# Performance work log

Hardware: AMD Instinct MI355X
Metric: run time of the kernel (lower is better)

## Reference

```python
import jax, jax.numpy as jnp
import numpy as np

B, T, DIM, H, HD = 2, 2048, 1024, 8, 128
ATTN_SCALE = 0.12  # attn_args.attn_scale (modded-nanogpt constant)
F32_EPS = float(np.finfo(np.float32).eps)  # F.rms_norm default eps


def ste_round(x):
    # straight-through round (round_grad_pt): identity gradient
    return x + jax.lax.stop_gradient(jnp.round(x) - x)


def quantized_linear(x, num_bits=8, eps=1e-5):
    num_steps = (2 ** num_bits - 1) // 2  # 127
    xnmin = jnp.minimum(jnp.min(x, -1, keepdims=True), -eps)
    xpmax = jnp.maximum(jnp.max(x, -1, keepdims=True), eps)
    xp = ste_round(x / xpmax * num_steps) / num_steps * xpmax
    xn = ste_round(x / xnmin * num_steps) / num_steps * xnmin
    return jnp.where(x >= 0, xp, xn)


def ternary_quantize_mean_special(w):
    # w: [3, hdim, dim]; per-leading-slice scale
    s = jnp.maximum(jnp.mean(jnp.mean(jnp.abs(w), -1, keepdims=True), -2, keepdims=True), 1e-5)
    return s * jnp.clip(ste_round(w / s), -1.0, 1.0)


def ternary_quantize(w):
    s = jnp.maximum(jnp.mean(jnp.abs(w)), 1e-5)
    return s * jnp.clip(ste_round(w / s), -1.0, 1.0)


def rmsnorm(x):
    return x * jax.lax.rsqrt(jnp.mean(x * x, -1, keepdims=True) + F32_EPS)


def rotary(x, cos, sin):
    # x: [B,T,H,HD]; cos,sin: [T, HD//2]
    x1, x2 = jnp.split(x, 2, axis=-1)
    c = cos[None, :, None, :]
    s = sin[None, :, None, :]
    return jnp.concatenate([x1 * c + x2 * s, -x1 * s + x2 * c], axis=-1)


def setup_inputs() -> dict:
    key = jax.random.key(0)
    ks = jax.random.split(key, 5)
    x = jax.random.normal(ks[0], (B, T, DIM), jnp.float32)
    ve = jax.random.normal(ks[1], (B, T, DIM), jnp.float32)
    sa_lambdas = jnp.array([0.5, 0.5], jnp.float32)
    inv_freq = 1.0 / (10000.0 ** (np.arange(0, HD, 2, dtype=np.float32) / HD))
    ang = np.arange(T, dtype=np.float32)[:, None] * inv_freq[None, :]
    cos = jnp.asarray(np.cos(ang), jnp.float32)
    sin = jnp.asarray(np.sin(ang), jnp.float32)
    bound = (3.0 ** 0.5) * 0.5 * DIM ** (-0.5)
    qkvo_w = jax.random.uniform(ks[2], (4, H * HD, DIM), jnp.float32, -bound, bound)
    gate_w = 0.1 * jax.random.normal(ks[3], (H, 12), jnp.float32)
    return {"x": x, "ve": ve, "sa_lambdas": sa_lambdas, "cos": cos, "sin": sin,
            "qkvo_w": qkvo_w, "gate_w": gate_w}


def reference(x, ve, sa_lambdas, cos, sin, qkvo_w, gate_w):
    # pre-activation int8 fake-quant (ENABLE_ATTN_PRE_ACT_QUANTIZATION)
    xq = quantized_linear(x, num_bits=8)
    # ternary-quantized QKV weights (ENABLE_ATTN_QUANTIZATION)
    w_qkv = ternary_quantize_mean_special(qkvo_w[:3]).reshape(3 * H * HD, DIM)
    qkv = jnp.einsum('btd,ed->bte', xq, w_qkv).reshape(B, T, 3 * H, HD)
    q, k, v = qkv[:, :, :H], qkv[:, :, H:2 * H], qkv[:, :, 2 * H:]
    q, k = rmsnorm(q), rmsnorm(k)
    q, k = rotary(q, cos, sin), rotary(k, cos, sin)
    v = sa_lambdas[0] * v + sa_lambdas[1] * ve.reshape(v.shape)
    # q/k int8 fake-quant (ENABLE_ATTN_ACT_QUANTIZATION)
    q = quantized_linear(q, num_bits=8)
    k = quantized_linear(k, num_bits=8)
    # causal SDPA with explicit scale
    scores = jnp.einsum('bqhd,bkhd->bhqk', q, k) * ATTN_SCALE
    mask = jnp.tril(jnp.ones((T, T), bool))
    scores = jnp.where(mask[None, None], scores, -jnp.inf)
    p = jax.nn.softmax(scores, axis=-1)
    y = jnp.einsum('bhqk,bkhd->bqhd', p, v)  # [B,T,H,HD]
    # sigmoid gate from first 12 features of (quantized) x
    gate = jax.nn.sigmoid(jnp.einsum('btf,hf->bth', xq[..., :12], gate_w))
    y = (y * gate[..., None]).reshape(B, T, H * HD)
    # ternary-quantized output projection (ENABLE_ATTN_PROJ_QUANTIZATION)
    w_o = ternary_quantize(qkvo_w[3])
    return jnp.einsum('bte,de->btd', y, w_o)
```

## Files before the change

kernel.cpp:

```cpp
#include <hip/hip_runtime.h>
#include <hip/hip_bf16.h>
#include <cstddef>
#include <cstdint>

#define B_    2
#define T_    2048
#define DIM_  1024
#define H_    8
#define HD_   128
#define BT_   (B_*T_)
#define E3_   (3*H_*HD_)
#define F32_EPS_ 1.1920929e-07f

typedef __attribute__((ext_vector_type(8))) short bh8_t;
typedef __attribute__((ext_vector_type(4))) float f32x4_t;
typedef __attribute__((ext_vector_type(16))) float f32x16_t;
typedef __attribute__((ext_vector_type(4))) unsigned short us4_t;

__device__ inline unsigned short bf16r(float f) {
    unsigned u = __builtin_bit_cast(unsigned, f);
    u = (u + 0x7fffu + ((u >> 16) & 1u)) >> 16;
    return (unsigned short)u;
}
__device__ inline unsigned bf16pk(float a, float b) {
    return (unsigned)bf16r(a) | ((unsigned)bf16r(b) << 16);
}
__device__ inline void gl16(const unsigned short* g, unsigned short* l) {
    __builtin_amdgcn_global_load_lds((const __attribute__((address_space(1))) void*)g,
                                     (__attribute__((address_space(3))) void*)l, 16, 0, 0);
}

__global__ __launch_bounds__(256) void absmean1_kernel(const float* __restrict__ w, float* __restrict__ partial) {
    int blk = blockIdx.x;
    size_t off = (size_t)blk * 4096;
    __shared__ float red[256];
    int tid = threadIdx.x;
    float acc = 0.f;
    const float* p = w + off + tid*16;
    #pragma unroll
    for (int j = 0; j < 4; j++) {
        float4 v = *(const float4*)(p + j*4);
        acc += fabsf(v.x) + fabsf(v.y) + fabsf(v.z) + fabsf(v.w);
    }
    red[tid] = acc; __syncthreads();
    for (int s = 128; s > 0; s >>= 1) { if (tid < s) red[tid] += red[tid+s]; __syncthreads(); }
    if (tid == 0) partial[blk] = red[0];
}

__global__ __launch_bounds__(256) void absmean2_kernel(const float* __restrict__ partial, float* __restrict__ scales) {
    int m = blockIdx.x;
    __shared__ float red[256];
    int tid = threadIdx.x;
    red[tid] = partial[m*256 + tid]; __syncthreads();
    for (int s = 128; s > 0; s >>= 1) { if (tid < s) red[tid] += red[tid+s]; __syncthreads(); }
    if (tid == 0) scales[m] = fmaxf(red[0] / (float)(DIM_*DIM_), 1e-5f);
}

__global__ __launch_bounds__(256) void quant_w_kernel(const float* __restrict__ w, const float* __restrict__ scales,
                                                      unsigned short* __restrict__ wq) {
    int base = (blockIdx.x * 256 + threadIdx.x) * 8;
    float s = scales[base >> 20];
    float inv = 1.f / s;
    unsigned short out[8];
    float4 v0 = *(const float4*)(w + base);
    float4 v1 = *(const float4*)(w + base + 4);
    float t[8] = {v0.x, v0.y, v0.z, v0.w, v1.x, v1.y, v1.z, v1.w};
    #pragma unroll
    for (int j = 0; j < 8; j++) {
        float r = rintf(t[j] * inv);
        r = fminf(1.f, fmaxf(-1.f, r));
        out[j] = (r == 0.f) ? 0 : (r > 0.f ? 0x3F80 : 0xBF80);
    }
    *(int4*)(wq + base) = *(const int4*)out;
}

__global__ __launch_bounds__(256) void quant_x_gate_kernel(const float* __restrict__ x, const float* __restrict__ gw,
                                                           unsigned short* __restrict__ xqb, float* __restrict__ gate) {
    int row = blockIdx.x;
    const float* xr = x + (size_t)row * DIM_;
    unsigned short* qr = xqb + (size_t)row * DIM_;
    __shared__ float red[256];
    __shared__ float x12[12];
    int tid = threadIdx.x;
    float v[4];
    float mn = 1e30f, mx = -1e30f;
    #pragma unroll
    for (int i = 0; i < 4; i++) {
        v[i] = xr[i*256 + tid];
        mn = fminf(mn, v[i]); mx = fmaxf(mx, v[i]);
    }
    red[tid] = mn; __syncthreads();
    for (int s = 128; s > 0; s >>= 1) { if (tid < s) red[tid] = fminf(red[tid], red[tid+s]); __syncthreads(); }
    mn = red[0]; __syncthreads();
    red[tid] = mx; __syncthreads();
    for (int s = 128; s > 0; s >>= 1) { if (tid < s) red[tid] = fmaxf(red[tid], red[tid+s]); __syncthreads(); }
    mx = red[0]; __syncthreads();
    float p = fmaxf(mx, 1e-5f);
    float n = fminf(mn, -1e-5f);
    #pragma unroll
    for (int i = 0; i < 4; i++) {
        int gi = i*256 + tid;
        float xv = v[i];
        float sc = (xv >= 0.f) ? p : n;
        float q = rintf(xv / sc * 127.f) / 127.f * sc;
        qr[gi] = bf16r(q);
        if (gi < 12) x12[gi] = q;
    }
    __syncthreads();
    if (tid < H_) {
        float acc = 0.f;
        #pragma unroll
        for (int f = 0; f < 12; f++) acc += x12[f] * gw[tid*12 + f];
        gate[(size_t)row * H_ + tid] = 1.f / (1.f + expf(-acc));
    }
}

__global__ __launch_bounds__(256) void gemm_bf16_kernel(const unsigned short* __restrict__ A,
                                                        const unsigned short* __restrict__ Bm,
                                                        const float* __restrict__ sw, int sbase,
                                                        float* __restrict__ C, int M, int N, int K) {
    __shared__ __align__(16) unsigned short As[128*64];
    __shared__ __align__(16) unsigned short Bs[128*64];
    int bm = blockIdx.y * 128, bn = blockIdx.x * 128;
    int tid = threadIdx.x;
    int w = tid >> 6, l = tid & 63;
    int wr = w >> 1, wc = w & 1;
    int lg = l >> 4, lq = l & 15;
    f32x4_t acc[4][4];
    #pragma unroll
    for (int mt = 0; mt < 4; mt++)
        #pragma unroll
        for (int nt = 0; nt < 4; nt++) acc[mt][nt] = (f32x4_t)0.f;

    for (int k0 = 0; k0 < K; k0 += 64) {
        #pragma unroll
        for (int i = 0; i < 4; i++) {
            int ob = (i*4 + w) << 10;
            int o  = ob + (l << 4);
            int row = o >> 7;
            int scn = (o >> 4) & 7;
            int lcn = scn ^ (row & 7);
            gl16(A  + (size_t)(bm+row)*K + k0 + lcn*8, (unsigned short*)As + (ob >> 1));
            gl16(Bm + (size_t)(bn+row)*K + k0 + lcn*8, (unsigned short*)Bs + (ob >> 1));
        }
        __syncthreads();
        #pragma unroll
        for (int kk = 0; kk < 2; kk++) {
            bh8_t af[4], bf[4];
            #pragma unroll
            for (int mt = 0; mt < 4; mt++) {
                int r = wr*64 + mt*16 + lq;
                int j = kk*4 + lg;
                af[mt] = *(const bh8_t*)(As + r*64 + (((j ^ (r & 7)))<<3));
            }
            #pragma unroll
            for (int nt = 0; nt < 4; nt++) {
                int r = wc*64 + nt*16 + lq;
                int j = kk*4 + lg;
                bf[nt] = *(const bh8_t*)(Bs + r*64 + (((j ^ (r & 7)))<<3));
            }
            #pragma unroll
            for (int mt = 0; mt < 4; mt++)
                #pragma unroll
                for (int nt = 0; nt < 4; nt++)
                    acc[mt][nt] = __builtin_amdgcn_mfma_f32_16x16x32_bf16(af[mt], bf[nt], acc[mt][nt], 0, 0, 0);
        }
        __syncthreads();
    }
    #pragma unroll
    for (int nt = 0; nt < 4; nt++) {
        int col = bn + wc*64 + nt*16 + lq;
        float s = sw[sbase + (col >> 10)];
        #pragma unroll
        for (int mt = 0; mt < 4; mt++) {
            int row = bm + wr*64 + mt*16 + lg*4;
            #pragma unroll
            for (int r = 0; r < 4; r++)
                C[(size_t)(row + r)*N + col] = acc[mt][nt][r] * s;
        }
    }
}

__global__ __launch_bounds__(256) void qkv_post_kernel(const float* __restrict__ qkv, const float* __restrict__ ve,
                                                       const float* __restrict__ lam,
                                                       const float* __restrict__ cosb, const float* __restrict__ sinb,
                                                       unsigned short* __restrict__ Qb, unsigned short* __restrict__ Kb,
                                                       unsigned short* __restrict__ Vb) {
    int bt = blockIdx.x;
    int b = bt >> 11, t = bt & (T_ - 1);
    int w = threadIdx.x >> 6, l = threadIdx.x & 63;
    const float* base = qkv + (size_t)bt * E3_;
    float l0 = lam[0], l1 = lam[1];
    #pragma unroll
    for (int i = 0; i < 2; i++) {
        int h = w*2 + i;
        const float* row = base + (16 + h)*HD_;
        const float* ver = ve + (size_t)bt*DIM_ + h*HD_;
        unsigned short* dst = Vb + ((size_t)(b*H_+h)*T_ + t)*HD_;
        dst[l]      = bf16r(l0*row[l]    + l1*ver[l]);
        dst[l + 64] = bf16r(l0*row[l+64] + l1*ver[l+64]);
    }
    float cc = cosb[(size_t)t*64 + l], ss = sinb[(size_t)t*64 + l];
    #pragma unroll
    for (int i = 0; i < 4; i++) {
        int part = w*4 + i;
        const float* row = base + part*HD_;
        float x1 = row[l], x2 = row[l+64];
        float ssq = x1*x1 + x2*x2;
        #pragma unroll
        for (int off = 1; off < 64; off <<= 1) ssq += __shfl_xor(ssq, off);
        float rms = 1.0f / sqrtf(ssq / 128.0f + F32_EPS_);
        x1 *= rms; x2 *= rms;
        float o1 = x1*cc + x2*ss;
        float o2 = -x1*ss + x2*cc;
        float mn = fminf(o1, o2), mx = fmaxf(o1, o2);
        #pragma unroll
        for (int off = 1; off < 64; off <<= 1) {
            mn = fminf(mn, __shfl_xor(mn, off));
            mx = fmaxf(mx, __shfl_xor(mx, off));
        }
        float p = fmaxf(mx, 1e-5f);
        float n = fminf(mn, -1e-5f);
        float s1 = (o1 >= 0.f) ? p : n;
        float s2 = (o2 >= 0.f) ? p : n;
        float q1 = rintf(o1 / s1 * 127.f) / 127.f * s1;
        float q2 = rintf(o2 / s2 * 127.f) / 127.f * s2;
        if (part < 8) {
            unsigned short* dst = Qb + ((size_t)(b*H_+part)*T_ + t)*HD_;
            dst[l] = bf16r(0.12f * q1); dst[l + 64] = bf16r(0.12f * q2);
        } else {
            unsigned short* dst = Kb + ((size_t)(b*H_+part-8)*T_ + t)*HD_;
            dst[l] = bf16r(q1); dst[l + 64] = bf16r(q2);
        }
    }
}

__global__ __launch_bounds__(256) void transpose_v_kernel(const unsigned short* __restrict__ Vb,
                                                          unsigned short* __restrict__ VT) {
    int tt = blockIdx.x;
    int dt = blockIdx.y;
    int bh = blockIdx.z;
    __shared__ unsigned short L[64][80];
    int tid = threadIdx.x;
    #pragma unroll
    for (int i = 0; i < 2; i++) {
        int c = tid + i*256;
        int r = c >> 3, dc = c & 7;
        int4 v = *(const int4*)(Vb + ((size_t)bh*T_ + tt*64 + r)*HD_ + dt*64 + dc*8);
        *(int4*)(&L[r][dc*8]) = v;
    }
    __syncthreads();
    #pragma unroll
    for (int i = 0; i < 2; i++) {
        int c = tid + i*256;
        int r = c >> 3, tc = c & 7;
        unsigned short tmp[8];
        #pragma unroll
        for (int jj = 0; jj < 8; jj++) tmp[jj] = L[tc*8+jj][r];
        *(int4*)(VT + ((size_t)bh*HD_ + dt*64 + r)*T_ + tt*64 + tc*8) = *(const int4*)tmp;
    }
}

__global__ __launch_bounds__(256) void attn_kernel(const unsigned short* __restrict__ Qb,
                                                   const unsigned short* __restrict__ Kb,
                                                   const unsigned short* __restrict__ VT,
                                                   const float* __restrict__ gate,
                                                   unsigned short* __restrict__ Yb) {
    __shared__ __align__(16) unsigned char SMEM[65536];
    int id = blockIdx.x;
    int bh = id & 15;
    int qi = id >> 4;
    int qt = (qi < 16) ? (31 - qi) : (qi - 16);
    int b = bh >> 3, h = bh & 7;
    int tid = threadIdx.x;
    int w = tid >> 6, l = tid & 63;
    int qsub = w >> 1, qq = w & 1;
    int hh = l >> 5, l5 = l & 31;
    int qrow = qsub*32 + l5;
    int qg = qt*64 + qrow;

    const unsigned short* Kbase = Kb + (size_t)bh*T_*HD_;
    const unsigned short* Vbase = VT + (size_t)bh*HD_*T_;
    const unsigned short* Qg = Qb + ((size_t)bh*T_ + (size_t)qt*64) * HD_;

    bh8_t qf[8];
    #pragma unroll
    for (int ks = 0; ks < 8; ks++)
        qf[ks] = *(const bh8_t*)(Qg + (size_t)qrow*HD_ + ks*16 + hh*8);

    int nr = qt + 1;

    f32x16_t o0 = (f32x16_t)0.f, o1 = (f32x16_t)0.f, o2 = (f32x16_t)0.f, o3 = (f32x16_t)0.f;
    float mrun = -1e20f, lrun = 0.f;

#define STAGE(BI, J) { \
    unsigned short* kb_ = (unsigned short*)(SMEM + (BI)*16384); \
    unsigned short* vb_ = (unsigned short*)(SMEM + 32768 + (BI)*16384); \
    _Pragma("unroll") \
    for (int i_ = 0; i_ < 4; i_++) { \
        int ob_ = (i_*4 + w) << 10; \
        int o_  = ob_ + (l << 4); \
        int rk_ = o_ >> 8; \
        int lk_ = ((o_ >> 4) & 15) ^ (rk_ & 7); \
        gl16(Kbase + (size_t)((J)*64 + rk_)*HD_ + lk_*8, kb_ + (ob_ >> 1)); \
        int rv_ = o_ >> 7; \
        int lv_ = ((o_ >> 4) & 7) ^ (rv_ & 7); \
        gl16(Vbase + (size_t)rv_*T_ + (J)*64 + lv_*8, vb_ + (ob_ >> 1)); \
    } }

    STAGE(0, 0);
    for (int j = 0; j < nr; j++) {
        if (j + 1 < nr) {
            STAGE((j+1) & 1, j+1);
            asm volatile("s_waitcnt vmcnt(8)" ::: "memory");
        } else {
            asm volatile("s_waitcnt vmcnt(0)" ::: "memory");
        }
        __builtin_amdgcn_s_barrier();
        asm volatile("" ::: "memory");
        const unsigned short* kb = (const unsigned short*)(SMEM + (j&1)*16384);
        const unsigned short* vb = (const unsigned short*)(SMEM + 32768 + (j&1)*16384);
        int kvb = j*64 + qq*32;
        if (kvb <= qt*64 + qsub*32 + 31) {
            f32x16_t s = (f32x16_t)0.f;
            int krow = qq*32 + l5;
            #pragma unroll
            for (int ks = 0; ks < 8; ks++) {
                int c = (ks*2 + hh) ^ (krow & 7);
                bh8_t kf = *(const bh8_t*)(kb + krow*128 + c*8);
                s = __builtin_amdgcn_mfma_f32_32x32x16_bf16(kf, qf[ks], s, 0, 0, 0);
            }
            if (kvb + 31 > qt*64 + qsub*32) {
                #pragma unroll
                for (int r = 0; r < 16; r++) {
                    int key = kvb + (r & 3) + 8*(r >> 2) + 4*hh;
                    if (key > qg) s[r] = -1e30f;
                }
            }
            float tm = s[0];
            #pragma unroll
            for (int r = 1; r < 16; r++) tm = fmaxf(tm, s[r]);
            tm = fmaxf(tm, __shfl_xor(tm, 32));
            if (!__all(tm - mrun <= 8.f)) {
                float mnew = fmaxf(mrun, tm);
                float scf = __expf(mrun - mnew);
                lrun *= scf;
                o0 *= scf; o1 *= scf; o2 *= scf; o3 *= scf;
                mrun = mnew;
            }
            float p[16]; float ls = 0.f;
            #pragma unroll
            for (int r = 0; r < 16; r++) { p[r] = __expf(s[r] - mrun); ls += p[r]; }
            ls += __shfl_xor(ls, 32);
            lrun += ls;
            unsigned u0 = bf16pk(p[0], p[1]),   u1 = bf16pk(p[2], p[3]);
            unsigned u2 = bf16pk(p[4], p[5]),   u3 = bf16pk(p[6], p[7]);
            unsigned u4 = bf16pk(p[8], p[9]),   u5 = bf16pk(p[10], p[11]);
            unsigned u6 = bf16pk(p[12], p[13]), u7 = bf16pk(p[14], p[15]);
            unsigned x0 = (unsigned)__shfl_xor((int)u0, 32), x1 = (unsigned)__shfl_xor((int)u1, 32);
            unsigned x2 = (unsigned)__shfl_xor((int)u2, 32), x3 = (unsigned)__shfl_xor((int)u3, 32);
            unsigned x4 = (unsigned)__shfl_xor((int)u4, 32), x5 = (unsigned)__shfl_xor((int)u5, 32);
            unsigned x6 = (unsigned)__shfl_xor((int)u6, 32), x7 = (unsigned)__shfl_xor((int)u7, 32);
            union { bh8_t v; unsigned uu[4]; } B0, B1;
            B0.uu[0] = hh ? x2 : u0;  B0.uu[1] = hh ? x3 : u1;
            B0.uu[2] = hh ? u2 : x0;  B0.uu[3] = hh ? u3 : x1;
            B1.uu[0] = hh ? x6 : u4;  B1.uu[1] = hh ? x7 : u5;
            B1.uu[2] = hh ? u6 : x4;  B1.uu[3] = hh ? u7 : x5;
#define PV_STEP(DT, OACC) { \
    int vrow = DT*32 + l5; \
    bh8_t vf0 = *(const bh8_t*)(vb + vrow*64 + (((qq*4 + hh) ^ (vrow & 7))<<3)); \
    OACC = __builtin_amdgcn_mfma_f32_32x32x16_bf16(vf0, B0.v, OACC, 0, 0, 0); \
    bh8_t vf1 = *(const bh8_t*)(vb + vrow*64 + (((qq*4 + 2 + hh) ^ (vrow & 7))<<3)); \
    OACC = __builtin_amdgcn_mfma_f32_32x32x16_bf16(vf1, B1.v, OACC, 0, 0, 0); }
            PV_STEP(0, o0) PV_STEP(1, o1) PV_STEP(2, o2) PV_STEP(3, o3)
#undef PV_STEP
        }
        asm volatile("s_waitcnt lgkmcnt(0)" ::: "memory");
        __builtin_amdgcn_s_barrier();
        asm volatile("" ::: "memory");
    }

    f32x16_t oA[4] = {o0, o1, o2, o3};
    float* OB = (float*)SMEM;
    float* ML = (float*)(SMEM + 32768);
    unsigned short* YS = (unsigned short*)(SMEM + 33280);
    if (qq != 0) {
        float* obuf = OB + (size_t)qsub * 4096;
        #pragma unroll
        for (int dt = 0; dt < 4; dt++)
            #pragma unroll
            for (int g = 0; g < 4; g++) {
                f32x4_t v4;
                #pragma unroll
                for (int e = 0; e < 4; e++) v4[e] = oA[dt][g*4+e];
                int ch = (dt*4 + g) ^ (l & 7);
                *(f32x4_t*)(obuf + l*64 + ch*4) = v4;
            }
        if (hh == 0) {
            ML[(qsub*32 + l5)*2]     = mrun;
            ML[(qsub*32 + l5)*2 + 1] = lrun;
        }
    }
    __syncthreads();
    if (qq == 0) {
        float mb = ML[(qsub*32 + l5)*2];
        float lb = ML[(qsub*32 + l5)*2 + 1];
        float mN = fmaxf(mrun, mb);
        float fa = __expf(mrun - mN), fb = __expf(mb - mN);
        const float* obuf = OB + (size_t)qsub * 4096;
        #pragma unroll
        for (int dt = 0; dt < 4; dt++)
            #pragma unroll
            for (int g = 0; g < 4; g++) {
                int ch = (dt*4 + g) ^ (l & 7);
                f32x4_t v4 = *(const f32x4_t*)(obuf + l*64 + ch*4);
                #pragma unroll
                for (int e = 0; e < 4; e++)
                    oA[dt][g*4+e] = oA[dt][g*4+e]*fa + v4[e]*fb;
            }
        lrun = lrun*fa + lb*fb;
        float gv = gate[((size_t)b*T_ + (size_t)qg)*H_ + h];
        float inv = gv / lrun;
        #pragma unroll
        for (int dt = 0; dt < 4; dt++)
            #pragma unroll
            for (int g = 0; g < 4; g++) {
                unsigned short pk4[4];
                #pragma unroll
                for (int e = 0; e < 4; e++) pk4[e] = bf16r(oA[dt][g*4+e] * inv);
                int ch = (dt*4 + g) ^ (qrow & 7);
                *(us4_t*)(YS + (size_t)qrow*128 + ch*8 + hh*4) = *(const us4_t*)pk4;
            }
    }
    __syncthreads();
    #pragma unroll
    for (int i = 0; i < 4; i++) {
        int idx = tid + i*256;
        int r = idx >> 4, scn = idx & 15;
        int lcn = scn ^ (r & 7);
        int4 v = *(const int4*)(YS + (size_t)r*128 + scn*8);
        *(int4*)(Yb + (size_t)(b*T_ + qt*64 + r)*DIM_ + h*HD_ + lcn*8) = v;
    }
#undef STAGE
}

extern "C" void kernel_launch(void* const* d_in, const int* in_sizes, int n_in,
                              void* d_out, int out_size, void* d_ws, size_t ws_size,
                              hipStream_t stream) {
    const float* x    = (const float*)d_in[0];
    const float* ve   = (const float*)d_in[1];
    const float* lam  = (const float*)d_in[2];
    const float* cosb = (const float*)d_in[3];
    const float* sinb = (const float*)d_in[4];
    const float* qkvo = (const float*)d_in[5];
    const float* gw   = (const float*)d_in[6];

    char* ws = (char*)d_ws;
    float* scales  = (float*)ws;
    float* partial = scales + 16;
    unsigned short* WQb = (unsigned short*)(ws + (1<<13));
    unsigned short* XQb = WQb + (size_t)4*DIM_*DIM_;
    float* QKV = (float*)(XQb + (size_t)BT_*DIM_);
    float* GT  = QKV + (size_t)BT_*E3_;
    unsigned short* Qb = (unsigned short*)(GT + (size_t)BT_*H_);
    unsigned short* Kb = Qb + (size_t)B_*H_*T_*HD_;
    unsigned short* VT = Kb + (size_t)B_*H_*T_*HD_;
    unsigned short* Vb = VT + (size_t)B_*H_*T_*HD_;
    unsigned short* Yb = (unsigned short*)QKV;

    absmean1_kernel<<<1024, 256, 0, stream>>>(qkvo, partial);
    absmean2_kernel<<<4, 256, 0, stream>>>(partial, scales);
    quant_w_kernel<<<(4*DIM_*DIM_)/(256*8), 256, 0, stream>>>(qkvo, scales, WQb);
    quant_x_gate_kernel<<<BT_, 256, 0, stream>>>(x, gw, XQb, GT);
    gemm_bf16_kernel<<<dim3(E3_/128, BT_/128), 256, 0, stream>>>(XQb, WQb, scales, 0, QKV, BT_, E3_, DIM_);
    qkv_post_kernel<<<BT_, 256, 0, stream>>>(QKV, ve, lam, cosb, sinb, Qb, Kb, Vb);
    transpose_v_kernel<<<dim3(T_/64, HD_/64, B_*H_), 256, 0, stream>>>(Vb, VT);
    attn_kernel<<<512, 256, 0, stream>>>(Qb, Kb, VT, GT, Yb);
    gemm_bf16_kernel<<<dim3(DIM_/128, BT_/128), 256, 0, stream>>>(Yb, WQb + (size_t)3*DIM_*DIM_, scales, 3,
                                                                  (float*)d_out, BT_, DIM_, DIM_);
}
```

Measured before the change: 152.5 us.

## Store QKV in bf16, use exp2 softmax, retile output GEMM, add setprio

The QKV GEMM now writes bf16 instead of fp32, which halves the intermediate traffic between it and the post-processing kernel. The attention softmax moves to exp2 by folding log2(e) into the Q scale, uses tree reductions and a hardware packed bf16 convert, and raises wave priority around the MFMA sections. The K LDS swizzle is widened to 16 chunks to reduce bank conflicts. The output projection uses 64-row tiles to launch more blocks. Rounding QKV to bf16 before the RMS norm adds precision loss.

Result: faster. 145.8 us (-4.4%).

```diff
diff --git a/kernel.cpp b/kernel.cpp
--- a/kernel.cpp
+++ b/kernel.cpp
@@ -11,6 +11,7 @@
 #define BT_   (B_*T_)
 #define E3_   (3*H_*HD_)
 #define F32_EPS_ 1.1920929e-07f
+#define QSC_  0.17312340490667562f
 
 typedef __attribute__((ext_vector_type(8))) short bh8_t;
 typedef __attribute__((ext_vector_type(4))) float f32x4_t;
@@ -22,8 +23,13 @@
     u = (u + 0x7fffu + ((u >> 16) & 1u)) >> 16;
     return (unsigned short)u;
 }
-__device__ inline unsigned bf16pk(float a, float b) {
-    return (unsigned)bf16r(a) | ((unsigned)bf16r(b) << 16);
+__device__ inline float b2f(unsigned short u) {
+    return __builtin_bit_cast(float, (unsigned)u << 16);
+}
+__device__ inline unsigned cvtpk(float a, float b) {
+    unsigned r;
+    asm("v_cvt_pk_bf16_f32 %0, %1, %2" : "=v"(r) : "v"(a), "v"(b));
+    return r;
 }
 __device__ inline void gl16(const unsigned short* g, unsigned short* l) {
     __builtin_amdgcn_global_load_lds((const __attribute__((address_space(1))) void*)g,
@@ -115,41 +121,48 @@
     }
 }
 
+template<int MT, bool OBF>
 __global__ __launch_bounds__(256) void gemm_bf16_kernel(const unsigned short* __restrict__ A,
                                                         const unsigned short* __restrict__ Bm,
                                                         const float* __restrict__ sw, int sbase,
-                                                        float* __restrict__ C, int M, int N, int K) {
-    __shared__ __align__(16) unsigned short As[128*64];
+                                                        void* __restrict__ Cv, int M, int N, int K) {
+    __shared__ __align__(16) unsigned short As[MT*32*64];
     __shared__ __align__(16) unsigned short Bs[128*64];
-    int bm = blockIdx.y * 128, bn = blockIdx.x * 128;
+    int bm = blockIdx.y * (MT*32), bn = blockIdx.x * 128;
     int tid = threadIdx.x;
     int w = tid >> 6, l = tid & 63;
     int wr = w >> 1, wc = w & 1;
     int lg = l >> 4, lq = l & 15;
-    f32x4_t acc[4][4];
-    #pragma unroll
-    for (int mt = 0; mt < 4; mt++)
+    f32x4_t acc[MT][4];
+    #pragma unroll
+    for (int mt = 0; mt < MT; mt++)
         #pragma unroll
         for (int nt = 0; nt < 4; nt++) acc[mt][nt] = (f32x4_t)0.f;
 
     for (int k0 = 0; k0 < K; k0 += 64) {
+        #pragma unroll
+        for (int i = 0; i < MT; i++) {
+            int ob = (i*4 + w) << 10;
+            int o  = ob + (l << 4);
+            int row = o >> 7;
+            int lcn = ((o >> 4) & 7) ^ (row & 7);
+            gl16(A + (size_t)(bm+row)*K + k0 + lcn*8, (unsigned short*)As + (ob >> 1));
+        }
         #pragma unroll
         for (int i = 0; i < 4; i++) {
             int ob = (i*4 + w) << 10;
             int o  = ob + (l << 4);
             int row = o >> 7;
-            int scn = (o >> 4) & 7;
-            int lcn = scn ^ (row & 7);
-            gl16(A  + (size_t)(bm+row)*K + k0 + lcn*8, (unsigned short*)As + (ob >> 1));
+            int lcn = ((o >> 4) & 7) ^ (row & 7);
             gl16(Bm + (size_t)(bn+row)*K + k0 + lcn*8, (unsigned short*)Bs + (ob >> 1));
         }
         __syncthreads();
         #pragma unroll
         for (int kk = 0; kk < 2; kk++) {
-            bh8_t af[4], bf[4];
-            #pragma unroll
-            for (int mt = 0; mt < 4; mt++) {
-                int r = wr*64 + mt*16 + lq;
+            bh8_t af[MT], bf[4];
+            #pragma unroll
+            for (int mt = 0; mt < MT; mt++) {
+                int r = wr*(MT*16) + mt*16 + lq;
                 int j = kk*4 + lg;
                 af[mt] = *(const bh8_t*)(As + r*64 + (((j ^ (r & 7)))<<3));
             }
@@ -160,7 +173,7 @@
                 bf[nt] = *(const bh8_t*)(Bs + r*64 + (((j ^ (r & 7)))<<3));
             }
             #pragma unroll
-            for (int mt = 0; mt < 4; mt++)
+            for (int mt = 0; mt < MT; mt++)
                 #pragma unroll
                 for (int nt = 0; nt < 4; nt++)
                     acc[mt][nt] = __builtin_amdgcn_mfma_f32_16x16x32_bf16(af[mt], bf[nt], acc[mt][nt], 0, 0, 0);
@@ -172,16 +185,21 @@
         int col = bn + wc*64 + nt*16 + lq;
         float s = sw[sbase + (col >> 10)];
         #pragma unroll
-        for (int mt = 0; mt < 4; mt++) {
-            int row = bm + wr*64 + mt*16 + lg*4;
-            #pragma unroll
-            for (int r = 0; r < 4; r++)
-                C[(size_t)(row + r)*N + col] = acc[mt][nt][r] * s;
-        }
-    }
-}
-
-__global__ __launch_bounds__(256) void qkv_post_kernel(const float* __restrict__ qkv, const float* __restrict__ ve,
+        for (int mt = 0; mt < MT; mt++) {
+            int row = bm + wr*(MT*16) + mt*16 + lg*4;
+            #pragma unroll
+            for (int r = 0; r < 4; r++) {
+                if constexpr (OBF)
+                    ((unsigned short*)Cv)[(size_t)(row + r)*N + col] = bf16r(acc[mt][nt][r] * s);
+                else
+                    ((float*)Cv)[(size_t)(row + r)*N + col] = acc[mt][nt][r] * s;
+            }
+        }
+    }
+}
+
+__global__ __launch_bounds__(256) void qkv_post_kernel(const unsigned short* __restrict__ qkvb,
+                                                       const float* __restrict__ ve,
                                                        const float* __restrict__ lam,
                                                        const float* __restrict__ cosb, const float* __restrict__ sinb,
                                                        unsigned short* __restrict__ Qb, unsigned short* __restrict__ Kb,
@@ -189,23 +207,23 @@
     int bt = blockIdx.x;
     int b = bt >> 11, t = bt & (T_ - 1);
     int w = threadIdx.x >> 6, l = threadIdx.x & 63;
-    const float* base = qkv + (size_t)bt * E3_;
+    const unsigned short* base = qkvb + (size_t)bt * E3_;
     float l0 = lam[0], l1 = lam[1];
     #pragma unroll
     for (int i = 0; i < 2; i++) {
         int h = w*2 + i;
-        const float* row = base + (16 + h)*HD_;
+        const unsigned short* row = base + (16 + h)*HD_;
         const float* ver = ve + (size_t)bt*DIM_ + h*HD_;
         unsigned short* dst = Vb + ((size_t)(b*H_+h)*T_ + t)*HD_;
-        dst[l]      = bf16r(l0*row[l]    + l1*ver[l]);
-        dst[l + 64] = bf16r(l0*row[l+64] + l1*ver[l+64]);
+        dst[l]      = bf16r(l0*b2f(row[l])    + l1*ver[l]);
+        dst[l + 64] = bf16r(l0*b2f(row[l+64]) + l1*ver[l+64]);
     }
     float cc = cosb[(size_t)t*64 + l], ss = sinb[(size_t)t*64 + l];
     #pragma unroll
     for (int i = 0; i < 4; i++) {
         int part = w*4 + i;
-        const float* row = base + part*HD_;
-        float x1 = row[l], x2 = row[l+64];
+        const unsigned short* row = base + part*HD_;
+        float x1 = b2f(row[l]), x2 = b2f(row[l+64]);
         float ssq = x1*x1 + x2*x2;
         #pragma unroll
         for (int off = 1; off < 64; off <<= 1) ssq += __shfl_xor(ssq, off);
@@ -227,7 +245,7 @@
         float q2 = rintf(o2 / s2 * 127.f) / 127.f * s2;
         if (part < 8) {
             unsigned short* dst = Qb + ((size_t)(b*H_+part)*T_ + t)*HD_;
-            dst[l] = bf16r(0.12f * q1); dst[l + 64] = bf16r(0.12f * q2);
+            dst[l] = bf16r(QSC_ * q1); dst[l + 64] = bf16r(QSC_ * q2);
         } else {
             unsigned short* dst = Kb + ((size_t)(b*H_+part-8)*T_ + t)*HD_;
             dst[l] = bf16r(q1); dst[l + 64] = bf16r(q2);
@@ -301,7 +319,7 @@
         int ob_ = (i_*4 + w) << 10; \
         int o_  = ob_ + (l << 4); \
         int rk_ = o_ >> 8; \
-        int lk_ = ((o_ >> 4) & 15) ^ (rk_ & 7); \
+        int lk_ = ((o_ >> 4) & 15) ^ (rk_ & 15); \
         gl16(Kbase + (size_t)((J)*64 + rk_)*HD_ + lk_*8, kb_ + (ob_ >> 1)); \
         int rv_ = o_ >> 7; \
         int lv_ = ((o_ >> 4) & 7) ^ (rv_ & 7); \
@@ -324,12 +342,14 @@
         if (kvb <= qt*64 + qsub*32 + 31) {
             f32x16_t s = (f32x16_t)0.f;
             int krow = qq*32 + l5;
+            __builtin_amdgcn_s_setprio(1);
             #pragma unroll
             for (int ks = 0; ks < 8; ks++) {
-                int c = (ks*2 + hh) ^ (krow & 7);
+                int c = (ks*2 + hh) ^ (krow & 15);
                 bh8_t kf = *(const bh8_t*)(kb + krow*128 + c*8);
                 s = __builtin_amdgcn_mfma_f32_32x32x16_bf16(kf, qf[ks], s, 0, 0, 0);
             }
+            __builtin_amdgcn_s_setprio(0);
             if (kvb + 31 > qt*64 + qsub*32) {
                 #pragma unroll
                 for (int r = 0; r < 16; r++) {
@@ -337,26 +357,34 @@
                     if (key > qg) s[r] = -1e30f;
                 }
             }
-            float tm = s[0];
-            #pragma unroll
-            for (int r = 1; r < 16; r++) tm = fmaxf(tm, s[r]);
+            float t8[8], t4[4];
+            #pragma unroll
+            for (int r = 0; r < 8; r++) t8[r] = fmaxf(s[2*r], s[2*r+1]);
+            #pragma unroll
+            for (int r = 0; r < 4; r++) t4[r] = fmaxf(t8[2*r], t8[2*r+1]);
+            float tm = fmaxf(fmaxf(t4[0], t4[1]), fmaxf(t4[2], t4[3]));
             tm = fmaxf(tm, __shfl_xor(tm, 32));
             if (!__all(tm - mrun <= 8.f)) {
                 float mnew = fmaxf(mrun, tm);
-                float scf = __expf(mrun - mnew);
+                float scf = __builtin_amdgcn_exp2f(mrun - mnew);
                 lrun *= scf;
                 o0 *= scf; o1 *= scf; o2 *= scf; o3 *= scf;
                 mrun = mnew;
             }
-            float p[16]; float ls = 0.f;
-            #pragma unroll
-            for (int r = 0; r < 16; r++) { p[r] = __expf(s[r] - mrun); ls += p[r]; }
+            float p[16];
+            #pragma unroll
+            for (int r = 0; r < 16; r++) p[r] = __builtin_amdgcn_exp2f(s[r] - mrun);
+            #pragma unroll
+            for (int r = 0; r < 8; r++) t8[r] = p[2*r] + p[2*r+1];
+            #pragma unroll
+            for (int r = 0; r < 4; r++) t4[r] = t8[2*r] + t8[2*r+1];
+            float ls = (t4[0] + t4[1]) + (t4[2] + t4[3]);
             ls += __shfl_xor(ls, 32);
             lrun += ls;
-            unsigned u0 = bf16pk(p[0], p[1]),   u1 = bf16pk(p[2], p[3]);
-            unsigned u2 = bf16pk(p[4], p[5]),   u3 = bf16pk(p[6], p[7]);
-            unsigned u4 = bf16pk(p[8], p[9]),   u5 = bf16pk(p[10], p[11]);
-            unsigned u6 = bf16pk(p[12], p[13]), u7 = bf16pk(p[14], p[15]);
+            unsigned u0 = cvtpk(p[0], p[1]),   u1 = cvtpk(p[2], p[3]);
+            unsigned u2 = cvtpk(p[4], p[5]),   u3 = cvtpk(p[6], p[7]);
+            unsigned u4 = cvtpk(p[8], p[9]),   u5 = cvtpk(p[10], p[11]);
+            unsigned u6 = cvtpk(p[12], p[13]), u7 = cvtpk(p[14], p[15]);
             unsigned x0 = (unsigned)__shfl_xor((int)u0, 32), x1 = (unsigned)__shfl_xor((int)u1, 32);
             unsigned x2 = (unsigned)__shfl_xor((int)u2, 32), x3 = (unsigned)__shfl_xor((int)u3, 32);
             unsigned x4 = (unsigned)__shfl_xor((int)u4, 32), x5 = (unsigned)__shfl_xor((int)u5, 32);
@@ -366,6 +394,7 @@
             B0.uu[2] = hh ? u2 : x0;  B0.uu[3] = hh ? u3 : x1;
             B1.uu[0] = hh ? x6 : u4;  B1.uu[1] = hh ? x7 : u5;
             B1.uu[2] = hh ? u6 : x4;  B1.uu[3] = hh ? u7 : x5;
+            __builtin_amdgcn_s_setprio(1);
 #define PV_STEP(DT, OACC) { \
     int vrow = DT*32 + l5; \
     bh8_t vf0 = *(const bh8_t*)(vb + vrow*64 + (((qq*4 + hh) ^ (vrow & 7))<<3)); \
@@ -374,6 +403,7 @@
     OACC = __builtin_amdgcn_mfma_f32_32x32x16_bf16(vf1, B1.v, OACC, 0, 0, 0); }
             PV_STEP(0, o0) PV_STEP(1, o1) PV_STEP(2, o2) PV_STEP(3, o3)
 #undef PV_STEP
+            __builtin_amdgcn_s_setprio(0);
         }
         asm volatile("s_waitcnt lgkmcnt(0)" ::: "memory");
         __builtin_amdgcn_s_barrier();
@@ -406,7 +436,7 @@
         float mb = ML[(qsub*32 + l5)*2];
         float lb = ML[(qsub*32 + l5)*2 + 1];
         float mN = fmaxf(mrun, mb);
-        float fa = __expf(mrun - mN), fb = __expf(mb - mN);
+        float fa = __builtin_amdgcn_exp2f(mrun - mN), fb = __builtin_amdgcn_exp2f(mb - mN);
         const float* obuf = OB + (size_t)qsub * 4096;
         #pragma unroll
         for (int dt = 0; dt < 4; dt++)
@@ -458,24 +488,24 @@
     char* ws = (char*)d_ws;
     float* scales  = (float*)ws;
     float* partial = scales + 16;
-    unsigned short* WQb = (unsigned short*)(ws + (1<<13));
-    unsigned short* XQb = WQb + (size_t)4*DIM_*DIM_;
-    float* QKV = (float*)(XQb + (size_t)BT_*DIM_);
-    float* GT  = QKV + (size_t)BT_*E3_;
+    unsigned short* WQb  = (unsigned short*)(ws + (1<<13));
+    unsigned short* XQb  = WQb + (size_t)4*DIM_*DIM_;
+    unsigned short* QKVb = XQb + (size_t)BT_*DIM_;
+    float* GT = (float*)(QKVb + (size_t)BT_*E3_);
     unsigned short* Qb = (unsigned short*)(GT + (size_t)BT_*H_);
     unsigned short* Kb = Qb + (size_t)B_*H_*T_*HD_;
     unsigned short* VT = Kb + (size_t)B_*H_*T_*HD_;
     unsigned short* Vb = VT + (size_t)B_*H_*T_*HD_;
-    unsigned short* Yb = (unsigned short*)QKV;
+    unsigned short* Yb = QKVb;
 
     absmean1_kernel<<<1024, 256, 0, stream>>>(qkvo, partial);
     absmean2_kernel<<<4, 256, 0, stream>>>(partial, scales);
     quant_w_kernel<<<(4*DIM_*DIM_)/(256*8), 256, 0, stream>>>(qkvo, scales, WQb);
     quant_x_gate_kernel<<<BT_, 256, 0, stream>>>(x, gw, XQb, GT);
-    gemm_bf16_kernel<<<dim3(E3_/128, BT_/128), 256, 0, stream>>>(XQb, WQb, scales, 0, QKV, BT_, E3_, DIM_);
-    qkv_post_kernel<<<BT_, 256, 0, stream>>>(QKV, ve, lam, cosb, sinb, Qb, Kb, Vb);
+    gemm_bf16_kernel<4, true><<<dim3(E3_/128, BT_/128), 256, 0, stream>>>(XQb, WQb, scales, 0, QKVb, BT_, E3_, DIM_);
+    qkv_post_kernel<<<BT_, 256, 0, stream>>>(QKVb, ve, lam, cosb, sinb, Qb, Kb, Vb);
     transpose_v_kernel<<<dim3(T_/64, HD_/64, B_*H_), 256, 0, stream>>>(Vb, VT);
     attn_kernel<<<512, 256, 0, stream>>>(Qb, Kb, VT, GT, Yb);
-    gemm_bf16_kernel<<<dim3(DIM_/128, BT_/128), 256, 0, stream>>>(Yb, WQb + (size_t)3*DIM_*DIM_, scales, 3,
-                                                                  (float*)d_out, BT_, DIM_, DIM_);
-}
+    gemm_bf16_kernel<2, false><<<dim3(DIM_/128, BT_/64), 256, 0, stream>>>(Yb, WQb + (size_t)3*DIM_*DIM_, scales, 3,
+                                                                           (float*)d_out, BT_, DIM_, DIM_);
+}
```
